# Performance work log

Hardware: AMD Instinct MI355X
Metric: run time of the kernel (lower is better)

Reference implementation:

```python
import jax, jax.numpy as jnp
import numpy as np
from math import sqrt

B, N, DIM_IN, DIM_K, DIM_V, NH = 4, 1024, 1024, 1024, 1024, 16


def setup_inputs() -> dict:
    key = jax.random.key(0)
    ks = jax.random.split(key, 5)
    x = jax.random.normal(ks[0], (B, N, DIM_IN), dtype=jnp.float32)
    y = jax.random.normal(ks[1], (B, N, DIM_IN), dtype=jnp.float32)
    # nn.Linear weights are (out_features, in_features); xavier-like scale
    s = 1.0 / sqrt(DIM_IN)
    Wq = jax.random.normal(ks[2], (DIM_K, DIM_IN), dtype=jnp.float32) * s
    Wk = jax.random.normal(ks[3], (DIM_K, DIM_IN), dtype=jnp.float32) * s
    Wv = jax.random.normal(ks[4], (DIM_V, DIM_IN), dtype=jnp.float32) * s
    return {"x": x, "y": y, "Wq": Wq, "Wk": Wk, "Wv": Wv}


def reference(x, y, Wq, Wk, Wv):
    b, n, _ = x.shape
    nh = NH
    dk = DIM_K // nh
    dv = DIM_V // nh
    norm = 1.0 / sqrt(dk)
    # project and split heads: (b, h, n, d)
    q = (x @ Wq.T).reshape(b, n, nh, dk).transpose(0, 2, 1, 3)
    k = (x @ Wk.T).reshape(b, n, nh, dk).transpose(0, 2, 1, 3)
    v = (y @ Wv.T).reshape(b, n, nh, dv).transpose(0, 2, 1, 3)
    scores = jnp.einsum("bhnd,bhmd->bhnm", q, k) * norm
    dist = jax.nn.softmax(scores, axis=-1)
    # contrast branch: softmax over (1 - dist)
    dist_a = jax.nn.softmax(1.0 - dist, axis=-1)
    c_att = jnp.einsum("bhnm,bhmd->bhnd", dist_a, v)
    c_att = c_att.transpose(0, 2, 1, 3).reshape(b, n, DIM_V)
    # normal branch: NOTE the original applies softmax to dist AGAIN
    dist2 = jax.nn.softmax(dist, axis=-1)
    att = jnp.einsum("bhnm,bhmd->bhnd", dist2, v)
    att = att.transpose(0, 2, 1, 3).reshape(b, n, DIM_V)
    return (c_att, att)
```

## Files before the change

kernel.cpp:

```cpp
#include <hip/hip_runtime.h>


typedef __attribute__((ext_vector_type(8))) short bf16x8;
typedef __attribute__((ext_vector_type(4))) float f32x4;
typedef __attribute__((ext_vector_type(4))) float float4v;
typedef __attribute__((ext_vector_type(2))) unsigned int uint2v;
typedef __attribute__((ext_vector_type(4))) unsigned short ushort4v;

#define DEVINL static __device__ __forceinline__

DEVINL unsigned f2bf_u(float f) {
  unsigned u = __float_as_uint(f);
  return (u + 0x7fffu + ((u >> 16) & 1u)) >> 16;
}
DEVINL unsigned short f2bf(float f) { return (unsigned short)f2bf_u(f); }
DEVINL unsigned pack2(float lo, float hi) { return f2bf_u(lo) | (f2bf_u(hi) << 16); }

DEVINL unsigned cvtpk(float lo, float hi) {
  unsigned r; asm("v_cvt_pk_bf16_f32 %0, %1, %2" : "=v"(r) : "v"(lo), "v"(hi)); return r;
}

DEVINL float fexp2(float x) {
  float r; asm("v_exp_f32 %0, %1" : "=v"(r) : "v"(x)); return r;
}

DEVINL void gload_lds16(const void* g, void* l) {
  __builtin_amdgcn_global_load_lds((const __attribute__((address_space(1))) unsigned int*)g,
                                   (__attribute__((address_space(3))) unsigned int*)l, 16, 0, 0);
}

DEVINL f32x4 mfma16(bf16x8 a, bf16x8 b, f32x4 c) {
  return __builtin_amdgcn_mfma_f32_16x16x32_bf16(a, b, c, 0, 0, 0);
}

DEVINL bf16x8 sq_frag(bf16x8 a) {
  union { bf16x8 h; unsigned u[4]; } ua; ua.h = a;
  union { unsigned u[4]; bf16x8 h; } ub;
#pragma unroll
  for (int d = 0; d < 4; ++d) {
    const float lo = __uint_as_float(ua.u[d] << 16);
    const float hi = __uint_as_float(ua.u[d] & 0xffff0000u);
    ub.u[d] = cvtpk(lo * lo, hi * hi);
  }
  return ub.h;
}

__global__ void cvt_all(const float* __restrict__ x, const float* __restrict__ y,
                        const float* __restrict__ wq, const float* __restrict__ wk,
                        const float* __restrict__ wv,
                        unsigned short* __restrict__ xb, unsigned short* __restrict__ yb,
                        unsigned short* __restrict__ wqb, unsigned short* __restrict__ wkb,
                        unsigned short* __restrict__ wvb) {
  long long e = (long long)blockIdx.x * 2048 + (long long)threadIdx.x * 8;
  const float* s; unsigned short* d; long long off;
  if (e < 4194304)       { s = x;  d = xb;  off = e; }
  else if (e < 8388608)  { s = y;  d = yb;  off = e - 4194304; }
  else if (e < 9437184)  { s = wq; d = wqb; off = e - 8388608; }
  else if (e < 10485760) { s = wk; d = wkb; off = e - 9437184; }
  else                   { s = wv; d = wvb; off = e - 10485760; }
  float4v a = *(const float4v*)(s + off);
  float4v b = *(const float4v*)(s + off + 4);
  ushort4v lo = { f2bf(a[0]), f2bf(a[1]), f2bf(a[2]), f2bf(a[3]) };
  ushort4v hi = { f2bf(b[0]), f2bf(b[1]), f2bf(b[2]), f2bf(b[3]) };
  *(ushort4v*)(d + off) = lo;
  *(ushort4v*)(d + off + 4) = hi;
}

__global__ __launch_bounds__(256, 3)
void gemm_proj(const unsigned short* __restrict__ xb, const unsigned short* __restrict__ yb,
               const unsigned short* __restrict__ wq, const unsigned short* __restrict__ wk,
               const unsigned short* __restrict__ wv,
               unsigned short* __restrict__ Qb, unsigned short* __restrict__ Kb,
               unsigned short* __restrict__ Vt) {
  const int z = blockIdx.z;
  const unsigned short* A  = (z == 2) ? yb : xb;
  const unsigned short* Bw = (z == 0) ? wq : ((z == 1) ? wk : wv);

  __shared__ unsigned short lA[128 * 32];
  __shared__ unsigned short lB[128 * 32];

  const int tid = threadIdx.x;
  const int w = tid >> 6, l = tid & 63;
  const int lq = l & 15, lg = l >> 4;
  const int tm = blockIdx.y, tn = blockIdx.x;

  const int srow = l >> 2;
  const int scol = (l & 3) * 8;
  const size_t arow0 = (size_t)tm * 128 + w * 16 + srow;
  const size_t brow0 = (size_t)tn * 128 + w * 16 + srow;
  const int wr = (w >> 1) * 64, wc = (w & 1) * 64;

  f32x4 zero4 = {0.f, 0.f, 0.f, 0.f};
  f32x4 acc[4][4];
#pragma unroll
  for (int m = 0; m < 4; ++m)
#pragma unroll
    for (int n = 0; n < 4; ++n) acc[m][n] = zero4;

  for (int k0 = 0; k0 < 1024; k0 += 32) {
    gload_lds16(A + arow0 * 1024 + k0 + scol,        &lA[w * 512]);
    gload_lds16(A + (arow0 + 64) * 1024 + k0 + scol, &lA[w * 512 + 2048]);
    gload_lds16(Bw + brow0 * 1024 + k0 + scol,        &lB[w * 512]);
    gload_lds16(Bw + (brow0 + 64) * 1024 + k0 + scol, &lB[w * 512 + 2048]);
    __syncthreads();
    bf16x8 af[4], bfr[4];
#pragma unroll
    for (int m = 0; m < 4; ++m) af[m]  = *(const bf16x8*)&lA[(wr + m * 16 + lq) * 32 + lg * 8];
#pragma unroll
    for (int n = 0; n < 4; ++n) bfr[n] = *(const bf16x8*)&lB[(wc + n * 16 + lq) * 32 + lg * 8];
#pragma unroll
    for (int m = 0; m < 4; ++m)
#pragma unroll
      for (int n = 0; n < 4; ++n)
        acc[m][n] = mfma16(af[m], bfr[n], acc[m][n]);
    __syncthreads();
  }

  if (z < 2) {
    unsigned short* O = (z == 0) ? Qb : Kb;
    const float scale = (z == 0) ? 0.18033688011116012f : 1.0f;
#pragma unroll
    for (int m = 0; m < 4; ++m)
#pragma unroll
      for (int n = 0; n < 4; ++n) {
        int row0 = tm * 128 + wr + m * 16 + lg * 4;
        int col  = tn * 128 + wc + n * 16 + lq;
#pragma unroll
        for (int j = 0; j < 4; ++j)
          O[(size_t)(row0 + j) * 1024 + col] = f2bf(acc[m][n][j] * scale);
      }
  } else {
#pragma unroll
    for (int m = 0; m < 4; ++m)
#pragma unroll
      for (int n = 0; n < 4; ++n) {
        int row0 = tm * 128 + wr + m * 16 + lg * 4;
        int col  = tn * 128 + wc + n * 16 + lq;
        int bb = row0 >> 10, n0 = row0 & 1023;
        uint2v p = { pack2(acc[m][n][0], acc[m][n][1]), pack2(acc[m][n][2], acc[m][n][3]) };
        *(uint2v*)(Vt + ((size_t)(bb * 1024 + col)) * 1024 + n0) = p;
      }
  }
}

DEVINL void stage_tileK(const unsigned short* __restrict__ ghead, int m0,
                        unsigned short* tile, int w, int l) {
#pragma unroll
  for (int i = 0; i < 2; ++i) {
    const int c = i * 256 + w * 64 + l;
    const int row = c >> 3;
    const int col16 = (c & 7) ^ (row & 7);
    gload_lds16(ghead + (size_t)(m0 + row) * 1024 + col16 * 8,
                tile + (size_t)(i * 256 + w * 64) * 8);
  }
}
DEVINL void stage_tileV(const unsigned short* __restrict__ ghead, int m0,
                        unsigned short* tile, int w, int l) {
#pragma unroll
  for (int i = 0; i < 2; ++i) {
    const int c = i * 256 + w * 64 + l;
    const int row = c >> 3;
    const int col16 = (c & 7) ^ (row & 7);
    gload_lds16(ghead + (size_t)row * 1024 + m0 + col16 * 8,
                tile + (size_t)(i * 256 + w * 64) * 8);
  }
}
DEVINL bf16x8 lds_rd(const unsigned short* tile, int r, int g) {
  return *(const bf16x8*)((const char*)tile + (r << 7) + ((g ^ (r & 7)) << 4));
}

__global__ __launch_bounds__(256, 2)
void attn_fused(const unsigned short* __restrict__ Qb, const unsigned short* __restrict__ Kb,
                const unsigned short* __restrict__ Vt, float* __restrict__ out) {
  __shared__ unsigned short Kl[2][4096];
  __shared__ unsigned short Vl[2][4096];
  __shared__ unsigned short Pl[4][2048];

  const int tid = threadIdx.x;
  const int w = tid >> 6, l = tid & 63;
  const int lq = l & 15, lg = l >> 4;

  const int orig = blockIdx.x;
  const int vid = (orig & 7) * 64 + (orig >> 3);
  const int tile = vid & 7;
  const int h = (vid >> 3) & 15;
  const int b = vid >> 7;
  const int qBase = tile * 128 + w * 32;

  const unsigned short* Khead = Kb + ((size_t)b << 20) + h * 64;
  const unsigned short* Vhead = Vt + ((size_t)(b * 1024 + h * 64)) * 1024;
  char* Pb = (char*)&Pl[w][0];

  bf16x8 qf[2][2];
#pragma unroll
  for (int qg = 0; qg < 2; ++qg)
#pragma unroll
    for (int kst = 0; kst < 2; ++kst)
      qf[qg][kst] = *(const bf16x8*)(Qb + ((size_t)(b * 1024 + qBase + qg * 16 + lq)) * 1024
                                        + h * 64 + kst * 32 + lg * 8);

  union { short s[8]; bf16x8 v; } onesU;
#pragma unroll
  for (int i = 0; i < 8; ++i) onesU.s[i] = (short)0x3F80;
  const bf16x8 ones = onesU.v;

  f32x4 zero4 = {0.f, 0.f, 0.f, 0.f};
  f32x4 m1[2][4], m2[2][4], mv[4];
  f32x4 s1a[2], s2a[2];
#pragma unroll
  for (int qg = 0; qg < 2; ++qg) {
    s1a[qg] = zero4; s2a[qg] = zero4;
#pragma unroll
    for (int dvg = 0; dvg < 4; ++dvg) { m1[qg][dvg] = zero4; m2[qg][dvg] = zero4; }
  }
#pragma unroll
  for (int dvg = 0; dvg < 4; ++dvg) mv[dvg] = zero4;

  stage_tileK(Khead, 0, Kl[0], w, l);
  stage_tileV(Vhead, 0, Vl[0], w, l);
  __syncthreads();

  for (int mc = 0; mc < 16; ++mc) {
    if (mc < 15) {
      stage_tileK(Khead, (mc + 1) * 64, Kl[(mc + 1) & 1], w, l);
      stage_tileV(Vhead, (mc + 1) * 64, Vl[(mc + 1) & 1], w, l);
    }
    const unsigned short* Kt  = Kl[mc & 1];
    const unsigned short* Vtl = Vl[mc & 1];

#pragma unroll
    for (int sub = 0; sub < 4; ++sub) {
      const int r = sub * 16 + lq;
      bf16x8 ka0 = lds_rd(Kt, r, lg);
      bf16x8 ka1 = lds_rd(Kt, r, 4 + lg);
      const int boff = lq * 128 + (((sub * 2 + (lg >> 1)) ^ (lq & 7)) << 4) + ((lg & 1) << 3);
#pragma unroll
      for (int qg = 0; qg < 2; ++qg) {
        f32x4 t = zero4;
        t = mfma16(ka0, qf[qg][0], t);
        t = mfma16(ka1, qf[qg][1], t);
        const float e0 = fexp2(fminf(t[0], 30.f)), e1 = fexp2(fminf(t[1], 30.f));
        const float e2 = fexp2(fminf(t[2], 30.f)), e3 = fexp2(fminf(t[3], 30.f));
        *(uint2v*)(Pb + qg * 2048 + boff) = (uint2v){ cvtpk(e0, e1), cvtpk(e2, e3) };
      }
    }

#pragma unroll
    for (int kst2 = 0; kst2 < 2; ++kst2) {
      bf16x8 vf[4];
#pragma unroll
      for (int dvg = 0; dvg < 4; ++dvg)
        vf[dvg] = lds_rd(Vtl, dvg * 16 + lq, kst2 * 4 + lg);
#pragma unroll
      for (int dvg = 0; dvg < 4; ++dvg)
        mv[dvg] = mfma16(ones, vf[dvg], mv[dvg]);
#pragma unroll
      for (int qg = 0; qg < 2; ++qg) {
        const int roff = qg * 2048 + lq * 128 + (((kst2 * 4 + lg) ^ (lq & 7)) << 4);
        bf16x8 a1 = *(const bf16x8*)(Pb + roff);
        bf16x8 a2 = sq_frag(a1);
        s1a[qg] = mfma16(a1, ones, s1a[qg]);
        s2a[qg] = mfma16(a2, ones, s2a[qg]);
#pragma unroll
        for (int dvg = 0; dvg < 4; ++dvg) {
          m1[qg][dvg] = mfma16(a1, vf[dvg], m1[qg][dvg]);
          m2[qg][dvg] = mfma16(a2, vf[dvg], m2[qg][dvg]);
        }
      }
    }
    __syncthreads();
  }

#pragma unroll
  for (int qg = 0; qg < 2; ++qg)
#pragma unroll
    for (int j = 0; j < 4; ++j) {
      const float Z  = s1a[qg][j];
      const float iZ = 1.0f / Z;
      const float c2 = 0.5f * iZ * iZ;
      const float S2c2 = c2 * s2a[qg][j];
      const float r2 = 1.0f / (1025.0f + S2c2);
      const float ra = 1.0f / (1023.0f + S2c2);
      const int nrow = qBase + qg * 16 + lg * 4 + j;
      const size_t rb = ((size_t)(b * 1024 + nrow)) * 1024 + h * 64;
#pragma unroll
      for (int dvg = 0; dvg < 4; ++dvg) {
        const int dv = dvg * 16 + lq;
        const float A0 = mv[dvg][j];
        const float A1 = m1[qg][dvg][j];
        const float A2 = m2[qg][dvg][j];
        const float num2 = A0 + iZ * A1 + c2 * A2;
        const float numa = A0 - iZ * A1 + c2 * A2;
        out[rb + dv] = numa * ra;
        out[4194304 + rb + dv] = num2 * r2;
      }
    }
}

extern "C" void kernel_launch(void* const* d_in, const int* in_sizes, int n_in,
                              void* d_out, int out_size, void* d_ws, size_t ws_size,
                              hipStream_t stream) {
  const float* x  = (const float*)d_in[0];
  const float* y  = (const float*)d_in[1];
  const float* Wq = (const float*)d_in[2];
  const float* Wk = (const float*)d_in[3];
  const float* Wv = (const float*)d_in[4];
  float* out = (float*)d_out;
  char* ws = (char*)d_ws;
  const size_t MB = 1024 * 1024;
  unsigned short* xb  = (unsigned short*)(ws + 0 * MB);
  unsigned short* yb  = (unsigned short*)(ws + 8 * MB);
  unsigned short* wqb = (unsigned short*)(ws + 16 * MB);
  unsigned short* wkb = (unsigned short*)(ws + 18 * MB);
  unsigned short* wvb = (unsigned short*)(ws + 20 * MB);
  unsigned short* Qb  = (unsigned short*)(ws + 22 * MB);
  unsigned short* Kb  = (unsigned short*)(ws + 30 * MB);
  unsigned short* Vt  = (unsigned short*)(ws + 38 * MB);

  cvt_all<<<dim3(5632), dim3(256), 0, stream>>>(x, y, Wq, Wk, Wv, xb, yb, wqb, wkb, wvb);

  gemm_proj<<<dim3(8, 32, 3), dim3(256), 0, stream>>>(xb, yb, wqb, wkb, wvb, Qb, Kb, Vt);

  attn_fused<<<dim3(512), dim3(256), 0, stream>>>(Qb, Kb, Vt, out);
}
```

Before: 93.44 us.

## Fuse fp32-to-bf16 conversion into projection GEMM and drop separate convert kernel

Removes the standalone conversion kernel and has the projection GEMM load fp32 inputs and weights directly into LDS. Fragments are converted to bf16 on the fly with packed conversion instructions, and the LDS layout uses an XOR swizzle to avoid bank conflicts. This saves one kernel launch and the write and re-read of bf16 copies of about 48MB of operands. In exchange the GEMM moves twice the bytes per tile from global memory, doubles its LDS footprint, and repeats the conversion work across tiles.

```diff
diff --git a/kernel.cpp b/kernel.cpp
--- a/kernel.cpp
+++ b/kernel.cpp
@@ -45,50 +45,48 @@
   return ub.h;
 }
 
-__global__ void cvt_all(const float* __restrict__ x, const float* __restrict__ y,
-                        const float* __restrict__ wq, const float* __restrict__ wk,
-                        const float* __restrict__ wv,
-                        unsigned short* __restrict__ xb, unsigned short* __restrict__ yb,
-                        unsigned short* __restrict__ wqb, unsigned short* __restrict__ wkb,
-                        unsigned short* __restrict__ wvb) {
-  long long e = (long long)blockIdx.x * 2048 + (long long)threadIdx.x * 8;
-  const float* s; unsigned short* d; long long off;
-  if (e < 4194304)       { s = x;  d = xb;  off = e; }
-  else if (e < 8388608)  { s = y;  d = yb;  off = e - 4194304; }
-  else if (e < 9437184)  { s = wq; d = wqb; off = e - 8388608; }
-  else if (e < 10485760) { s = wk; d = wkb; off = e - 9437184; }
-  else                   { s = wv; d = wvb; off = e - 10485760; }
-  float4v a = *(const float4v*)(s + off);
-  float4v b = *(const float4v*)(s + off + 4);
-  ushort4v lo = { f2bf(a[0]), f2bf(a[1]), f2bf(a[2]), f2bf(a[3]) };
-  ushort4v hi = { f2bf(b[0]), f2bf(b[1]), f2bf(b[2]), f2bf(b[3]) };
-  *(ushort4v*)(d + off) = lo;
-  *(ushort4v*)(d + off + 4) = hi;
+DEVINL bf16x8 frag_cvt(const float* tile, int r, int lg) {
+  const char* base = (const char*)tile + r * 128;
+  const int s0 = (2 * lg) ^ (r & 7);
+  const int s1 = s0 ^ 1;
+  f32x4 a = *(const f32x4*)(base + s0 * 16);
+  f32x4 bb = *(const f32x4*)(base + s1 * 16);
+  union { unsigned u[4]; bf16x8 h; } ub;
+  ub.u[0] = cvtpk(a[0], a[1]);
+  ub.u[1] = cvtpk(a[2], a[3]);
+  ub.u[2] = cvtpk(bb[0], bb[1]);
+  ub.u[3] = cvtpk(bb[2], bb[3]);
+  return ub.h;
 }
 
 __global__ __launch_bounds__(256, 3)
-void gemm_proj(const unsigned short* __restrict__ xb, const unsigned short* __restrict__ yb,
-               const unsigned short* __restrict__ wq, const unsigned short* __restrict__ wk,
-               const unsigned short* __restrict__ wv,
+void gemm_proj(const float* __restrict__ x, const float* __restrict__ y,
+               const float* __restrict__ Wq, const float* __restrict__ Wk,
+               const float* __restrict__ Wv,
                unsigned short* __restrict__ Qb, unsigned short* __restrict__ Kb,
                unsigned short* __restrict__ Vt) {
   const int z = blockIdx.z;
-  const unsigned short* A  = (z == 2) ? yb : xb;
-  const unsigned short* Bw = (z == 0) ? wq : ((z == 1) ? wk : wv);
-
-  __shared__ unsigned short lA[128 * 32];
-  __shared__ unsigned short lB[128 * 32];
+  const float* A  = (z == 2) ? y : x;
+  const float* Bw = (z == 0) ? Wq : ((z == 1) ? Wk : Wv);
+
+  __shared__ float lA[128 * 32];
+  __shared__ float lB[128 * 32];
 
   const int tid = threadIdx.x;
   const int w = tid >> 6, l = tid & 63;
   const int lq = l & 15, lg = l >> 4;
   const int tm = blockIdx.y, tn = blockIdx.x;
-
-  const int srow = l >> 2;
-  const int scol = (l & 3) * 8;
-  const size_t arow0 = (size_t)tm * 128 + w * 16 + srow;
-  const size_t brow0 = (size_t)tn * 128 + w * 16 + srow;
   const int wr = (w >> 1) * 64, wc = (w & 1) * 64;
+
+  int srow[4], scol[4];
+#pragma unroll
+  for (int i = 0; i < 4; ++i) {
+    const int c = i * 256 + tid;
+    srow[i] = c >> 3;
+    scol[i] = ((c & 7) ^ ((c >> 3) & 7)) * 4;
+  }
+  const size_t aBase = (size_t)tm * 128 * 1024;
+  const size_t bBase = (size_t)tn * 128 * 1024;
 
   f32x4 zero4 = {0.f, 0.f, 0.f, 0.f};
   f32x4 acc[4][4];
@@ -98,16 +96,19 @@
     for (int n = 0; n < 4; ++n) acc[m][n] = zero4;
 
   for (int k0 = 0; k0 < 1024; k0 += 32) {
-    gload_lds16(A + arow0 * 1024 + k0 + scol,        &lA[w * 512]);
-    gload_lds16(A + (arow0 + 64) * 1024 + k0 + scol, &lA[w * 512 + 2048]);
-    gload_lds16(Bw + brow0 * 1024 + k0 + scol,        &lB[w * 512]);
-    gload_lds16(Bw + (brow0 + 64) * 1024 + k0 + scol, &lB[w * 512 + 2048]);
+#pragma unroll
+    for (int i = 0; i < 4; ++i) {
+      gload_lds16(A  + aBase + (size_t)srow[i] * 1024 + k0 + scol[i],
+                  lA + (i * 256 + w * 64) * 4);
+      gload_lds16(Bw + bBase + (size_t)srow[i] * 1024 + k0 + scol[i],
+                  lB + (i * 256 + w * 64) * 4);
+    }
     __syncthreads();
     bf16x8 af[4], bfr[4];
 #pragma unroll
-    for (int m = 0; m < 4; ++m) af[m]  = *(const bf16x8*)&lA[(wr + m * 16 + lq) * 32 + lg * 8];
-#pragma unroll
-    for (int n = 0; n < 4; ++n) bfr[n] = *(const bf16x8*)&lB[(wc + n * 16 + lq) * 32 + lg * 8];
+    for (int m = 0; m < 4; ++m) af[m]  = frag_cvt(lA, wr + m * 16 + lq, lg);
+#pragma unroll
+    for (int n = 0; n < 4; ++n) bfr[n] = frag_cvt(lB, wc + n * 16 + lq, lg);
 #pragma unroll
     for (int m = 0; m < 4; ++m)
 #pragma unroll
@@ -308,18 +309,11 @@
   float* out = (float*)d_out;
   char* ws = (char*)d_ws;
   const size_t MB = 1024 * 1024;
-  unsigned short* xb  = (unsigned short*)(ws + 0 * MB);
-  unsigned short* yb  = (unsigned short*)(ws + 8 * MB);
-  unsigned short* wqb = (unsigned short*)(ws + 16 * MB);
-  unsigned short* wkb = (unsigned short*)(ws + 18 * MB);
-  unsigned short* wvb = (unsigned short*)(ws + 20 * MB);
   unsigned short* Qb  = (unsigned short*)(ws + 22 * MB);
   unsigned short* Kb  = (unsigned short*)(ws + 30 * MB);
   unsigned short* Vt  = (unsigned short*)(ws + 38 * MB);
 
-  cvt_all<<<dim3(5632), dim3(256), 0, stream>>>(x, y, Wq, Wk, Wv, xb, yb, wqb, wkb, wvb);
-
-  gemm_proj<<<dim3(8, 32, 3), dim3(256), 0, stream>>>(xb, yb, wqb, wkb, wvb, Qb, Kb, Vt);
+  gemm_proj<<<dim3(8, 32, 3), dim3(256), 0, stream>>>(x, y, Wq, Wk, Wv, Qb, Kb, Vt);
 
   attn_fused<<<dim3(512), dim3(256), 0, stream>>>(Qb, Kb, Vt, out);
 }
```

Result: no change. 94.34 us (+1.0%).
